# Kernel optimization log

Hardware: AMD Instinct MI355X
Metric: run time of the kernel (lower is better)

## Reference

```python
import jax, jax.numpy as jnp
import numpy as np

MARGIN = 0.5


def _pairwise_sqdist(a, b):
    # ||a_i - b_j||^2 = |a_i|^2 + |b_j|^2 - 2 a_i . b_j  -> [N, N]
    a2 = jnp.sum(a * a, axis=1)
    b2 = jnp.sum(b * b, axis=1)
    return a2[:, None] + b2[None, :] - 2.0 * (a @ b.T)


def setup_inputs() -> dict:
    key = jax.random.key(0)
    k1, k2 = jax.random.split(key)
    N, D = 4096, 256
    pair1 = jax.random.normal(k1, (N, D), dtype=jnp.float32)
    pair2 = jax.random.normal(k2, (N, D), dtype=jnp.float32)
    return {"pair1": pair1, "pair2": pair2}


def reference(pair1, pair2):
    N = pair1.shape[0]
    d11 = _pairwise_sqdist(pair1, pair1)          # dist(p1_i, p1_j)
    d12 = _pairwise_sqdist(pair1, pair2)          # dist(p1_i, p2_j)
    dist_ap = jnp.diagonal(d12)                   # ||p1_i - p2_i||^2, [N]
    off_diag = 1.0 - jnp.eye(N, dtype=pair1.dtype)  # exclude j == i
    hinge = (jax.nn.relu(dist_ap[:, None] - d11 + MARGIN)
             + jax.nn.relu(dist_ap[:, None] - d12 + MARGIN))
    losses = jnp.sum(hinge * off_diag)
    cnt = N * (N - 1)
    return losses / cnt
```

## Files before the change

kernel.cpp:

```cpp
#include <hip/hip_runtime.h>

#define NN 4096
#define DD 256
#define MARGIN 0.5f

typedef __attribute__((ext_vector_type(8))) short bf16x8;
typedef __attribute__((ext_vector_type(4))) float f32x4;

__device__ inline unsigned short f32_to_bf16_rne(float v) {
    unsigned int b = __float_as_uint(v);
    b += 0x7FFFu + ((b >> 16) & 1u);
    return (unsigned short)(b >> 16);
}
__device__ inline float bf16_to_f32(unsigned short u) {
    return __uint_as_float(((unsigned int)u) << 16);
}

__global__ __launch_bounds__(256) void stats_convert(
    const float* __restrict__ p1, const float* __restrict__ p2,
    unsigned short* __restrict__ pb, float* __restrict__ nb,
    float* __restrict__ ai, float* __restrict__ corr)
{
    const int wave = threadIdx.x >> 6;
    const int lane = threadIdx.x & 63;
    const int row  = blockIdx.x * 4 + wave;

    const float4 x = *(const float4*)&p1[(size_t)row * DD + lane * 4];
    const float4 y = *(const float4*)&p2[(size_t)row * DD + lane * 4];

    ushort4 xb, yb;
    xb.x = f32_to_bf16_rne(x.x); xb.y = f32_to_bf16_rne(x.y);
    xb.z = f32_to_bf16_rne(x.z); xb.w = f32_to_bf16_rne(x.w);
    yb.x = f32_to_bf16_rne(y.x); yb.y = f32_to_bf16_rne(y.y);
    yb.z = f32_to_bf16_rne(y.z); yb.w = f32_to_bf16_rne(y.w);
    *(ushort4*)&pb[(size_t)row * DD + lane * 4] = xb;
    *(ushort4*)&pb[(size_t)(NN + row) * DD + lane * 4] = yb;

    float s1 = x.x*x.x + x.y*x.y + x.z*x.z + x.w*x.w;
    float s2 = y.x*y.x + y.y*y.y + y.z*y.z + y.w*y.w;
    float dx = x.x-y.x, dy = x.y-y.y, dz = x.z-y.z, dw = x.w-y.w;
    float sa = dx*dx + dy*dy + dz*dz + dw*dw;

    float xf0 = bf16_to_f32(xb.x), xf1 = bf16_to_f32(xb.y),
          xf2 = bf16_to_f32(xb.z), xf3 = bf16_to_f32(xb.w);
    float yf0 = bf16_to_f32(yb.x), yf1 = bf16_to_f32(yb.y),
          yf2 = bf16_to_f32(yb.z), yf3 = bf16_to_f32(yb.w);
    float s1b  = xf0*xf0 + xf1*xf1 + xf2*xf2 + xf3*xf3;
    float s12b = xf0*yf0 + xf1*yf1 + xf2*yf2 + xf3*yf3;

    #pragma unroll
    for (int off = 32; off > 0; off >>= 1) {
        s1  += __shfl_down(s1,  off);
        s2  += __shfl_down(s2,  off);
        sa  += __shfl_down(sa,  off);
        s1b += __shfl_down(s1b, off);
        s12b+= __shfl_down(s12b,off);
    }
    if (lane == 0) {
        nb[row]      = s1;
        nb[NN + row] = s2;
        ai[row]      = sa - s1 + MARGIN;
        const float t1 = fmaxf(sa - 2.f*s1 + MARGIN + 2.f*s1b, 0.f);
        const float t2 = fmaxf(sa - s1 - s2 + MARGIN + 2.f*s12b, 0.f);
        corr[row] = t1 + t2;
    }
}

__global__ __launch_bounds__(256, 2) void gemm_hinge(
    const unsigned short* __restrict__ pb,
    const float* __restrict__ nb, const float* __restrict__ ai,
    float* __restrict__ partial)
{
    __shared__ unsigned short Bs[2][64 * 256];
    __shared__ float wsum[4];

    const int t    = threadIdx.x;
    const int lane = t & 63;
    const int wave = t >> 6;
    const int wm   = wave >> 1;
    const int wn   = wave & 1;

    const int bid     = blockIdx.x;
    const int istripe = (bid & 7) * 4 + (bid >> 7);
    const int jgroup  = (bid >> 3) & 15;
    const int i0      = istripe * 128;
    const int jt0     = jgroup * 8;

    const int lr = lane & 15;
    const int l4 = lane >> 4;
    const int lk = l4 * 8;

    auto stage = [&](int sel, int jt) {
        const unsigned short* base = pb + (size_t)jt * 64 * DD;
        #pragma unroll
        for (int q = 0; q < 8; ++q) {
            const int c   = q * 256 + t;
            const int row = c >> 5;
            const int cw  = c & 31;
            const unsigned short* g = base + row * DD + ((cw ^ (row & 7)) * 8);
            __builtin_amdgcn_global_load_lds(
                (const __attribute__((address_space(1))) unsigned int*)g,
                (__attribute__((address_space(3))) unsigned int*)
                    &Bs[sel][(q * 256 + wave * 64) * 8],
                16, 0, 0);
        }
    };

    stage(0, jt0 + 0);

    bf16x8 a[4][8];
    #pragma unroll
    for (int m = 0; m < 4; ++m) {
        const unsigned short* ar = pb + (size_t)(i0 + wm * 64 + m * 16 + lr) * DD + lk;
        #pragma unroll
        for (int kq = 0; kq < 8; ++kq)
            a[m][kq] = *(const bf16x8*)(ar + kq * 32);
    }

    const int r0 = l4 * 4;
    float aiv[4][4];
    #pragma unroll
    for (int m = 0; m < 4; ++m)
        #pragma unroll
        for (int r = 0; r < 4; ++r)
            aiv[m][r] = ai[i0 + wm * 64 + m * 16 + r0 + r];

    float nbv[8][2];
    #pragma unroll
    for (int jj = 0; jj < 8; ++jj)
        #pragma unroll
        for (int n = 0; n < 2; ++n)
            nbv[jj][n] = nb[jgroup * 512 + jj * 64 + wn * 32 + n * 16 + lr];

    stage(1, jt0 + 1);

    asm volatile("s_waitcnt vmcnt(8)" ::: "memory");
    __builtin_amdgcn_sched_barrier(0);
    __builtin_amdgcn_s_barrier();
    __builtin_amdgcn_sched_barrier(0);

    float lsum = 0.f;

    for (int jj = 0; jj < 8; ++jj) {
        const int sel = jj & 1;

        f32x4 acc[4][2];
        #pragma unroll
        for (int m = 0; m < 4; ++m)
            #pragma unroll
            for (int n = 0; n < 2; ++n)
                acc[m][n] = (f32x4){0.f, 0.f, 0.f, 0.f};

        __builtin_amdgcn_s_setprio(1);
        #pragma unroll
        for (int kq = 0; kq < 8; ++kq) {
            bf16x8 b[2];
            #pragma unroll
            for (int n = 0; n < 2; ++n) {
                const int row = wn * 32 + n * 16 + lr;
                const int cl  = kq * 4 + l4;
                b[n] = *(const bf16x8*)&Bs[sel][row * 256 + ((cl ^ (row & 7)) * 8)];
            }
            #pragma unroll
            for (int m = 0; m < 4; ++m)
                #pragma unroll
                for (int n = 0; n < 2; ++n)
                    acc[m][n] = __builtin_amdgcn_mfma_f32_16x16x32_bf16(
                        a[m][kq], b[n], acc[m][n], 0, 0, 0);
        }
        __builtin_amdgcn_s_setprio(0);

        #pragma unroll
        for (int n = 0; n < 2; ++n) {
            const float nbj = nbv[jj][n];
            #pragma unroll
            for (int m = 0; m < 4; ++m)
                #pragma unroll
                for (int r = 0; r < 4; ++r)
                    lsum += fmaxf(fmaf(2.f, acc[m][n][r], aiv[m][r] - nbj), 0.f);
        }

        if (jj < 6) {
            __builtin_amdgcn_s_barrier();
            __builtin_amdgcn_sched_barrier(0);
            stage(sel, jt0 + jj + 2);
            asm volatile("s_waitcnt vmcnt(8)" ::: "memory");
            __builtin_amdgcn_sched_barrier(0);
            __builtin_amdgcn_s_barrier();
            __builtin_amdgcn_sched_barrier(0);
        } else if (jj == 6) {
            asm volatile("s_waitcnt vmcnt(0)" ::: "memory");
            __builtin_amdgcn_sched_barrier(0);
            __builtin_amdgcn_s_barrier();
            __builtin_amdgcn_sched_barrier(0);
        }
    }

    #pragma unroll
    for (int off = 32; off > 0; off >>= 1) lsum += __shfl_down(lsum, off);
    if (lane == 0) wsum[wave] = lsum;
    __syncthreads();
    if (t == 0)
        partial[bid] = wsum[0] + wsum[1] + wsum[2] + wsum[3];
}

__global__ __launch_bounds__(256) void final_reduce(
    const float* __restrict__ partial, const float* __restrict__ corr,
    float* __restrict__ out, float scale)
{
    const int t = threadIdx.x;
    float s = 0.f;
    for (int i = t; i < 512; i += 256) s += partial[i];
    for (int i = t; i < NN; i += 256) s -= corr[i];
    #pragma unroll
    for (int off = 32; off > 0; off >>= 1) s += __shfl_down(s, off);
    __shared__ float w[4];
    if ((t & 63) == 0) w[t >> 6] = s;
    __syncthreads();
    if (t == 0) out[0] = (w[0] + w[1] + w[2] + w[3]) * scale;
}

extern "C" void kernel_launch(void* const* d_in, const int* in_sizes, int n_in,
                              void* d_out, int out_size, void* d_ws, size_t ws_size,
                              hipStream_t stream) {
    const float* p1 = (const float*)d_in[0];
    const float* p2 = (const float*)d_in[1];
    float* out = (float*)d_out;

    char* ws = (char*)d_ws;
    unsigned short* pb = (unsigned short*)ws;
    float* nb      = (float*)(ws + (size_t)2 * NN * DD * 2);
    float* ai      = nb + 2 * NN;
    float* corr    = ai + NN;
    float* partial = corr + NN;
    const float scale = 1.0f / ((float)NN * (float)(NN - 1));

    stats_convert<<<NN / 4, 256, 0, stream>>>(p1, p2, pb, nb, ai, corr);
    gemm_hinge<<<512, 256, 0, stream>>>(pb, nb, ai, partial);
    final_reduce<<<1, 256, 0, stream>>>(partial, corr, out, scale);
}
```

Baseline: 39.04 us.

## Restructure B-tile pipeline with single-stage prefetch and register double-buffering

Each iteration now issues the next tile's global-to-LDS load at its top, into the buffer not being read. A __syncthreads at the end of the iteration replaces the hand-placed vmcnt waits and split barriers. Inside the k-loop, B fragments are read from LDS one step ahead into registers so that LDS reads can overlap the MFMAs, and the s_setprio hints are dropped. The simpler synchronisation waits for the in-flight tile every iteration, so load latency is hidden only by a single iteration's compute rather than by the previous two-tile-ahead scheme.

```diff
diff --git a/kernel.cpp b/kernel.cpp
--- a/kernel.cpp
+++ b/kernel.cpp
@@ -106,7 +106,7 @@
         }
     };
 
-    stage(0, jt0 + 0);
+    stage(0, jt0);
 
     bf16x8 a[4][8];
     #pragma unroll
@@ -132,17 +132,13 @@
         for (int n = 0; n < 2; ++n)
             nbv[jj][n] = nb[jgroup * 512 + jj * 64 + wn * 32 + n * 16 + lr];
 
-    stage(1, jt0 + 1);
-
-    asm volatile("s_waitcnt vmcnt(8)" ::: "memory");
-    __builtin_amdgcn_sched_barrier(0);
-    __builtin_amdgcn_s_barrier();
-    __builtin_amdgcn_sched_barrier(0);
+    __syncthreads();
 
     float lsum = 0.f;
+    int sel = 0;
 
     for (int jj = 0; jj < 8; ++jj) {
-        const int sel = jj & 1;
+        if (jj < 7) stage(sel ^ 1, jt0 + jj + 1);
 
         f32x4 acc[4][2];
         #pragma unroll
@@ -151,24 +147,32 @@
             for (int n = 0; n < 2; ++n)
                 acc[m][n] = (f32x4){0.f, 0.f, 0.f, 0.f};
 
-        __builtin_amdgcn_s_setprio(1);
+        bf16x8 bcur[2], bnxt[2];
+        #pragma unroll
+        for (int n = 0; n < 2; ++n) {
+            const int row = wn * 32 + n * 16 + lr;
+            bcur[n] = *(const bf16x8*)&Bs[sel][row * 256 + ((l4 ^ (row & 7)) * 8)];
+        }
         #pragma unroll
         for (int kq = 0; kq < 8; ++kq) {
-            bf16x8 b[2];
-            #pragma unroll
-            for (int n = 0; n < 2; ++n) {
-                const int row = wn * 32 + n * 16 + lr;
-                const int cl  = kq * 4 + l4;
-                b[n] = *(const bf16x8*)&Bs[sel][row * 256 + ((cl ^ (row & 7)) * 8)];
+            if (kq < 7) {
+                #pragma unroll
+                for (int n = 0; n < 2; ++n) {
+                    const int row = wn * 32 + n * 16 + lr;
+                    const int cl  = (kq + 1) * 4 + l4;
+                    bnxt[n] = *(const bf16x8*)
+                        &Bs[sel][row * 256 + ((cl ^ (row & 7)) * 8)];
+                }
             }
             #pragma unroll
             for (int m = 0; m < 4; ++m)
                 #pragma unroll
                 for (int n = 0; n < 2; ++n)
                     acc[m][n] = __builtin_amdgcn_mfma_f32_16x16x32_bf16(
-                        a[m][kq], b[n], acc[m][n], 0, 0, 0);
-        }
-        __builtin_amdgcn_s_setprio(0);
+                        a[m][kq], bcur[n], acc[m][n], 0, 0, 0);
+            #pragma unroll
+            for (int n = 0; n < 2; ++n) bcur[n] = bnxt[n];
+        }
 
         #pragma unroll
         for (int n = 0; n < 2; ++n) {
@@ -180,20 +184,8 @@
                     lsum += fmaxf(fmaf(2.f, acc[m][n][r], aiv[m][r] - nbj), 0.f);
         }
 
-        if (jj < 6) {
-            __builtin_amdgcn_s_barrier();
-            __builtin_amdgcn_sched_barrier(0);
-            stage(sel, jt0 + jj + 2);
-            asm volatile("s_waitcnt vmcnt(8)" ::: "memory");
-            __builtin_amdgcn_sched_barrier(0);
-            __builtin_amdgcn_s_barrier();
-            __builtin_amdgcn_sched_barrier(0);
-        } else if (jj == 6) {
-            asm volatile("s_waitcnt vmcnt(0)" ::: "memory");
-            __builtin_amdgcn_sched_barrier(0);
-            __builtin_amdgcn_s_barrier();
-            __builtin_amdgcn_sched_barrier(0);
-        }
+        __syncthreads();
+        sel ^= 1;
     }
 
     #pragma unroll
```

After: 55.20 us. 41.4% more time.
